# Optimization experiments

Hardware: AMD Instinct MI355X
Metric: run time of the kernel (lower is better)

## Reference

```python
import jax, jax.numpy as jnp
import numpy as np

NUM_HEADS = 16


def spike(x):
    # forward of SpikeFunction: Heaviside step
    return (x > 0).astype(x.dtype)


def setup_inputs() -> dict:
    key = jax.random.key(0)
    ks = jax.random.split(key, 11)
    B, S, D = 2, 2048, 1024
    s = 1.0 / np.sqrt(D)
    return {
        "query": jax.random.normal(ks[0], (B, S, D), jnp.float32),
        "key": jax.random.normal(ks[1], (B, S, D), jnp.float32),
        "value": jax.random.normal(ks[2], (B, S, D), jnp.float32),
        "Wq": jax.random.normal(ks[3], (D, D), jnp.float32) * s,
        "bq": jnp.zeros((D,), jnp.float32),
        "Wk": jax.random.normal(ks[4], (D, D), jnp.float32) * s,
        "bk": jnp.zeros((D,), jnp.float32),
        "Wv": jax.random.normal(ks[5], (D, D), jnp.float32) * s,
        "bv": jnp.zeros((D,), jnp.float32),
        "Wo": jax.random.normal(ks[6], (D, D), jnp.float32) * s,
        "bo": jnp.zeros((D,), jnp.float32),
    }


def reference(query, key, value, Wq, bq, Wk, bk, Wv, bv, Wo, bo):
    B, S, D = query.shape
    H = NUM_HEADS
    hd = D // H
    # torch Linear: x @ W.T + b
    q = (query @ Wq.T + bq).reshape(B, S, H, hd).transpose(0, 2, 1, 3)
    k = (key @ Wk.T + bk).reshape(B, S, H, hd).transpose(0, 2, 1, 3)
    v = (value @ Wv.T + bv).reshape(B, S, H, hd).transpose(0, 2, 1, 3)
    scale = 1.0 / np.sqrt(hd).astype(np.float32)
    scores = jnp.einsum('bhqd,bhkd->bhqk', q, k) * scale  # [B,H,S,S]
    attn = spike(scores)  # elementwise threshold instead of softmax
    ctx = jnp.einsum('bhqk,bhkd->bhqd', attn, v)
    ctx = ctx.transpose(0, 2, 1, 3).reshape(B, S, D)
    out = ctx @ Wo.T + bo
    return out, attn
```

## Files before the change

### kernel.cpp

```cpp
#include <hip/hip_runtime.h>


#define SEQ 2048
#define DIM 1024
#define NH 16
#define HD 64
#define BATCH 2
#define MROWS (BATCH * SEQ)
#define BHT (BATCH * NH)

typedef __attribute__((ext_vector_type(8))) short short8;
typedef __attribute__((ext_vector_type(4))) float f4;
typedef unsigned short ushort;

__device__ __forceinline__ f4 mfma16(short8 a, short8 b, f4 c) {
    return __builtin_amdgcn_mfma_f32_16x16x32_bf16(a, b, c, 0, 0, 0);
}
__device__ __forceinline__ ushort rne16(float x) {
    union { float f; unsigned u; } a; a.f = x;
    return (ushort)((a.u + 0x7fffu + ((a.u >> 16) & 1u)) >> 16);
}
__device__ __forceinline__ void split2(float x, ushort& h, ushort& l) {
    union { float f; unsigned u; } a; a.f = x;
    unsigned hu = a.u & 0xffff0000u;
    h = (ushort)(hu >> 16);
    union { unsigned u; float f; } hb; hb.u = hu;
    l = rne16(x - hb.f);
}
__device__ __forceinline__ short8 ld8(const ushort* p) { return *(const short8*)p; }

__device__ __forceinline__ void gll16(const ushort* g, ushort* l) {
    __builtin_amdgcn_global_load_lds((const __attribute__((address_space(1))) void*)g,
                                     (__attribute__((address_space(3))) void*)l, 16, 0, 0);
}

__global__ __launch_bounds__(256) void wconv(const float* __restrict__ Wq,
                                             const float* __restrict__ Wk,
                                             const float* __restrict__ Wv,
                                             const float* __restrict__ Wo,
                                             ushort* __restrict__ Wqh, ushort* __restrict__ Wql,
                                             ushort* __restrict__ Wkh, ushort* __restrict__ Wkl,
                                             ushort* __restrict__ Wvb, ushort* __restrict__ Wob) {
    int i = (blockIdx.x * 256 + threadIdx.x) * 4;
    int job = blockIdx.y;
    const float* src = job == 0 ? Wq : job == 1 ? Wk : job == 2 ? Wv : Wo;
    float4 w = *(const float4*)&src[i];
    float xs[4] = {w.x, w.y, w.z, w.w};
    if (job < 2) {
        ushort h[4], l[4];
#pragma unroll
        for (int j = 0; j < 4; ++j) split2(xs[j], h[j], l[j]);
        ushort* ph = job ? Wkh : Wqh;
        ushort* pl = job ? Wkl : Wql;
        *(short4*)&ph[i] = make_short4(h[0], h[1], h[2], h[3]);
        *(short4*)&pl[i] = make_short4(l[0], l[1], l[2], l[3]);
    } else {
        ushort* po = job == 2 ? Wvb : Wob;
        *(short4*)&po[i] = make_short4(rne16(xs[0]), rne16(xs[1]), rne16(xs[2]), rne16(xs[3]));
    }
}

template <int B>
__device__ __forceinline__ void ld_qk(const float* __restrict__ X, const ushort* __restrict__ Wh,
                                      const ushort* __restrict__ Wl, int m0, int n0, int la, int qd,
                                      int k0, float4 (&xA)[2][2][2], short8 (&wH)[2][4],
                                      short8 (&wL)[2][4]) {
#pragma unroll
    for (int ms = 0; ms < 2; ++ms) {
        const float* ap = &X[(size_t)(m0 + ms * 16 + la) * DIM + k0 + qd * 8];
        xA[B][ms][0] = *(const float4*)ap;
        xA[B][ms][1] = *(const float4*)(ap + 4);
    }
#pragma unroll
    for (int ns = 0; ns < 4; ++ns) {
        size_t wi = (size_t)(n0 + ns * 16 + la) * DIM + k0 + qd * 8;
        wH[B][ns] = ld8(&Wh[wi]);
        wL[B][ns] = ld8(&Wl[wi]);
    }
}

template <int B>
__device__ __forceinline__ void fma_qk(float4 (&xA)[2][2][2], short8 (&wH)[2][4],
                                       short8 (&wL)[2][4], f4 (&acc)[2][4]) {
    short8 ahi[2], alo[2];
#pragma unroll
    for (int ms = 0; ms < 2; ++ms) {
        float xs[8] = {xA[B][ms][0].x, xA[B][ms][0].y, xA[B][ms][0].z, xA[B][ms][0].w,
                       xA[B][ms][1].x, xA[B][ms][1].y, xA[B][ms][1].z, xA[B][ms][1].w};
#pragma unroll
        for (int j = 0; j < 8; ++j) {
            ushort h, l;
            split2(xs[j], h, l);
            ahi[ms][j] = (short)h;
            alo[ms][j] = (short)l;
        }
    }
#pragma unroll
    for (int ns = 0; ns < 4; ++ns)
#pragma unroll
        for (int ms = 0; ms < 2; ++ms) {
            acc[ms][ns] = mfma16(alo[ms], wH[B][ns], acc[ms][ns]);
            acc[ms][ns] = mfma16(ahi[ms], wL[B][ns], acc[ms][ns]);
            acc[ms][ns] = mfma16(ahi[ms], wH[B][ns], acc[ms][ns]);
        }
}

template <int B>
__device__ __forceinline__ void ld_v(const float* __restrict__ X, const ushort* __restrict__ Wb,
                                     int m0, int n0, int la, int qd, int k0,
                                     float4 (&xA)[2][2][2], short8 (&wH)[2][4]) {
#pragma unroll
    for (int ms = 0; ms < 2; ++ms) {
        const float* ap = &X[(size_t)(m0 + ms * 16 + la) * DIM + k0 + qd * 8];
        xA[B][ms][0] = *(const float4*)ap;
        xA[B][ms][1] = *(const float4*)(ap + 4);
    }
#pragma unroll
    for (int ns = 0; ns < 4; ++ns)
        wH[B][ns] = ld8(&Wb[(size_t)(n0 + ns * 16 + la) * DIM + k0 + qd * 8]);
}

template <int B>
__device__ __forceinline__ void fma_v(float4 (&xA)[2][2][2], short8 (&wH)[2][4], f4 (&acc)[2][4]) {
    short8 a[2];
#pragma unroll
    for (int ms = 0; ms < 2; ++ms) {
        float xs[8] = {xA[B][ms][0].x, xA[B][ms][0].y, xA[B][ms][0].z, xA[B][ms][0].w,
                       xA[B][ms][1].x, xA[B][ms][1].y, xA[B][ms][1].z, xA[B][ms][1].w};
#pragma unroll
        for (int j = 0; j < 8; ++j) a[ms][j] = (short)rne16(xs[j]);
    }
#pragma unroll
    for (int ns = 0; ns < 4; ++ns)
#pragma unroll
        for (int ms = 0; ms < 2; ++ms) acc[ms][ns] = mfma16(a[ms], wH[B][ns], acc[ms][ns]);
}

__global__ __launch_bounds__(256, 2) void proj_qkv(
    const float* __restrict__ query, const float* __restrict__ key, const float* __restrict__ value,
    const ushort* __restrict__ Wqh, const ushort* __restrict__ Wql,
    const ushort* __restrict__ Wkh, const ushort* __restrict__ Wkl,
    const ushort* __restrict__ Wvb,
    const float* __restrict__ bq, const float* __restrict__ bk, const float* __restrict__ bv,
    ushort* __restrict__ Qhi, ushort* __restrict__ Qlo,
    ushort* __restrict__ Khi, ushort* __restrict__ Klo, ushort* __restrict__ Vt) {
    const int z = blockIdx.z;
    const int t = threadIdx.x, wave = t >> 6, lane = t & 63;
    const int la = lane & 15, qd = lane >> 4;
    const int m0 = blockIdx.x * 128 + wave * 32;
    const int n0 = blockIdx.y * 64;

    float4 xA[2][2][2];
    short8 wH[2][4], wL[2][4];
    f4 acc[2][4] = {};

    if (z < 2) {
        const float* X = z ? key : query;
        const ushort* Wh = z ? Wkh : Wqh;
        const ushort* Wl = z ? Wkl : Wql;
        ld_qk<0>(X, Wh, Wl, m0, n0, la, qd, 0, xA, wH, wL);
        for (int k0 = 0; k0 < DIM; k0 += 64) {
            ld_qk<1>(X, Wh, Wl, m0, n0, la, qd, k0 + 32, xA, wH, wL);
            fma_qk<0>(xA, wH, wL, acc);
            ld_qk<0>(X, Wh, Wl, m0, n0, la, qd, (k0 + 64) & (DIM - 1), xA, wH, wL);
            fma_qk<1>(xA, wH, wL, acc);
        }
        const float* bias = z ? bk : bq;
        ushort* Oh = z ? Khi : Qhi;
        ushort* Ol = z ? Klo : Qlo;
#pragma unroll
        for (int ns = 0; ns < 4; ++ns) {
            int n = n0 + ns * 16 + la;
            float bvv = bias[n];
            int h = n >> 6, d = n & 63;
#pragma unroll
            for (int ms = 0; ms < 2; ++ms)
#pragma unroll
                for (int r = 0; r < 4; ++r) {
                    int m = m0 + ms * 16 + qd * 4 + r;
                    int b = m >> 11, s = m & 2047;
                    ushort hh, ll;
                    split2(acc[ms][ns][r] + bvv, hh, ll);
                    size_t o = ((size_t)(b * NH + h) * SEQ + s) * HD + d;
                    __builtin_nontemporal_store(hh, &Oh[o]);
                    __builtin_nontemporal_store(ll, &Ol[o]);
                }
        }
    } else {
        __shared__ ushort Ts[4][64][40];
        ld_v<0>(value, Wvb, m0, n0, la, qd, 0, xA, wH);
        for (int k0 = 0; k0 < DIM; k0 += 64) {
            ld_v<1>(value, Wvb, m0, n0, la, qd, k0 + 32, xA, wH);
            fma_v<0>(xA, wH, acc);
            ld_v<0>(value, Wvb, m0, n0, la, qd, (k0 + 64) & (DIM - 1), xA, wH);
            fma_v<1>(xA, wH, acc);
        }
#pragma unroll
        for (int ns = 0; ns < 4; ++ns) {
            float bvv = bv[n0 + ns * 16 + la];
#pragma unroll
            for (int ms = 0; ms < 2; ++ms)
#pragma unroll
                for (int r = 0; r < 4; ++r)
                    Ts[wave][ns * 16 + la][ms * 16 + qd * 4 + r] = rne16(acc[ms][ns][r] + bvv);
        }
        int b = m0 >> 11, s0 = m0 & 2047, h = n0 >> 6;
        size_t vbase = (size_t)(b * NH + h) * HD * SEQ;
#pragma unroll
        for (int it = 0; it < 4; ++it) {
            int d = it * 16 + (lane >> 2), sc = (lane & 3) * 8;
            short8 v0 = *(const short8*)&Ts[wave][d][sc];
            __builtin_nontemporal_store(v0, (short8*)&Vt[vbase + (size_t)d * SEQ + s0 + sc]);
        }
    }
}

__global__ __launch_bounds__(256, 4) void attn_mfma(
    const ushort* __restrict__ Qhi, const ushort* __restrict__ Qlo,
    const ushort* __restrict__ Khi, const ushort* __restrict__ Klo,
    const ushort* __restrict__ Vt, float* __restrict__ attn, ushort* __restrict__ ctxb) {
    __shared__ ushort kb[2][2][32][64];
    __shared__ ushort Ps[64][40];
    const int t = threadIdx.x, wave = t >> 6, lane = t & 63;
    const int la = lane & 15, qd = lane >> 4;
    const int bh = blockIdx.x;
    const int q0 = blockIdx.y * 64 + wave * 16;

    short8 qhi[2], qlo[2];
#pragma unroll
    for (int ks = 0; ks < 2; ++ks) {
        size_t qi = ((size_t)bh * SEQ + q0 + la) * HD + ks * 32 + qd * 8;
        qhi[ks] = ld8(&Qhi[qi]);
        qlo[ks] = ld8(&Qlo[qi]);
    }

    const int skey = wave * 8 + (lane >> 3);
    const int schunk = (lane & 7) ^ (lane >> 3);
    const size_t sgbase = ((size_t)bh * SEQ + skey) * HD + schunk * 8;

    gll16(&Khi[sgbase], &kb[0][0][wave * 8][0]);
    gll16(&Klo[sgbase], &kb[0][1][wave * 8][0]);
    __syncthreads();

    f4 cacc[4] = {};
    for (int h = 0; h < 64; ++h) {
        const int c0 = h * 32;
        const int cur = h & 1;

        short8 vB[4];
#pragma unroll
        for (int ns = 0; ns < 4; ++ns)
            vB[ns] = ld8(&Vt[((size_t)bh * HD + ns * 16 + la) * SEQ + c0 + qd * 8]);

        if (h + 1 < 64) {
            gll16(&Khi[sgbase + (size_t)(c0 + 32) * HD], &kb[cur ^ 1][0][wave * 8][0]);
            gll16(&Klo[sgbase + (size_t)(c0 + 32) * HD], &kb[cur ^ 1][1][wave * 8][0]);
        }

        short8 kH[2][2], kL[2][2];
#pragma unroll
        for (int n2 = 0; n2 < 2; ++n2)
#pragma unroll
            for (int ks = 0; ks < 2; ++ks) {
                int row = n2 * 16 + la;
                int sw = ((ks * 4 + qd) ^ (la & 7)) * 8;
                kH[n2][ks] = *(const short8*)&kb[cur][0][row][sw];
                kL[n2][ks] = *(const short8*)&kb[cur][1][row][sw];
            }

        f4 s[2] = {};
        __builtin_amdgcn_s_setprio(1);
#pragma unroll
        for (int n2 = 0; n2 < 2; ++n2)
#pragma unroll
            for (int ks = 0; ks < 2; ++ks) {
                s[n2] = mfma16(qlo[ks], kH[n2][ks], s[n2]);
                s[n2] = mfma16(qhi[ks], kL[n2][ks], s[n2]);
                s[n2] = mfma16(qhi[ks], kH[n2][ks], s[n2]);
            }
        __builtin_amdgcn_s_setprio(0);

#pragma unroll
        for (int n2 = 0; n2 < 2; ++n2)
#pragma unroll
            for (int r = 0; r < 4; ++r)
                Ps[wave * 16 + qd * 4 + r][n2 * 16 + la] =
                    s[n2][r] > 0.f ? (ushort)0x3f80 : (ushort)0;

#pragma unroll
        for (int it = 0; it < 2; ++it) {
            int row = it * 8 + (lane >> 3);
            short4 p = *(const short4*)&Ps[wave * 16 + row][(lane & 7) * 4];
            f4 o;
            o.x = __uint_as_float(((unsigned)(ushort)p.x) << 16);
            o.y = __uint_as_float(((unsigned)(ushort)p.y) << 16);
            o.z = __uint_as_float(((unsigned)(ushort)p.z) << 16);
            o.w = __uint_as_float(((unsigned)(ushort)p.w) << 16);
            __builtin_nontemporal_store(
                o, (f4*)&attn[((size_t)bh * SEQ + q0 + row) * SEQ + c0 + (lane & 7) * 4]);
        }

        short8 pa = *(const short8*)&Ps[wave * 16 + la][qd * 8];
        __builtin_amdgcn_s_setprio(1);
#pragma unroll
        for (int ns = 0; ns < 4; ++ns) cacc[ns] = mfma16(pa, vB[ns], cacc[ns]);
        __builtin_amdgcn_s_setprio(0);

        __syncthreads();
    }
#pragma unroll
    for (int ns = 0; ns < 4; ++ns)
#pragma unroll
        for (int r = 0; r < 4; ++r) {
            int qrow = q0 + qd * 4 + r;
            __builtin_nontemporal_store(rne16(cacc[ns][r]),
                                        &ctxb[((size_t)bh * SEQ + qrow) * HD + ns * 16 + la]);
        }
}

template <int B>
__device__ __forceinline__ void ld_o(const ushort* __restrict__ Ctx, const ushort* __restrict__ Wb,
                                     int m0, int n0, int la, int qd, int k0,
                                     short8 (&aO)[2][2], short8 (&wO)[2][4]) {
#pragma unroll
    for (int ms = 0; ms < 2; ++ms) {
        int m = m0 + ms * 16 + la;
        int b = m >> 11, s = m & 2047;
        int k = k0 + qd * 8;
        int h = k >> 6, d = k & 63;
        aO[B][ms] = ld8(&Ctx[((size_t)(b * NH + h) * SEQ + s) * HD + d]);
    }
#pragma unroll
    for (int ns = 0; ns < 4; ++ns)
        wO[B][ns] = ld8(&Wb[(size_t)(n0 + ns * 16 + la) * DIM + k0 + qd * 8]);
}

__global__ __launch_bounds__(256, 2) void proj_out(const ushort* __restrict__ Ctx,
                                                   const ushort* __restrict__ Wb,
                                                   const float* __restrict__ bias,
                                                   float* __restrict__ out) {
    const int t = threadIdx.x, wave = t >> 6, lane = t & 63;
    const int la = lane & 15, qd = lane >> 4;
    const int m0 = blockIdx.x * 128 + wave * 32;
    const int n0 = blockIdx.y * 64;

    short8 aO[2][2], wO[2][4];
    f4 acc[2][4] = {};
    ld_o<0>(Ctx, Wb, m0, n0, la, qd, 0, aO, wO);
    for (int k0 = 0; k0 < DIM; k0 += 64) {
        ld_o<1>(Ctx, Wb, m0, n0, la, qd, k0 + 32, aO, wO);
#pragma unroll
        for (int ns = 0; ns < 4; ++ns)
#pragma unroll
            for (int ms = 0; ms < 2; ++ms) acc[ms][ns] = mfma16(aO[0][ms], wO[0][ns], acc[ms][ns]);
        ld_o<0>(Ctx, Wb, m0, n0, la, qd, (k0 + 64) & (DIM - 1), aO, wO);
#pragma unroll
        for (int ns = 0; ns < 4; ++ns)
#pragma unroll
            for (int ms = 0; ms < 2; ++ms) acc[ms][ns] = mfma16(aO[1][ms], wO[1][ns], acc[ms][ns]);
    }
#pragma unroll
    for (int ns = 0; ns < 4; ++ns) {
        int n = n0 + ns * 16 + la;
        float bvv = bias[n];
#pragma unroll
        for (int ms = 0; ms < 2; ++ms)
#pragma unroll
            for (int r = 0; r < 4; ++r) {
                int m = m0 + ms * 16 + qd * 4 + r;
                __builtin_nontemporal_store(acc[ms][ns][r] + bvv, &out[(size_t)m * DIM + n]);
            }
    }
}

extern "C" void kernel_launch(void* const* d_in, const int* in_sizes, int n_in,
                              void* d_out, int out_size, void* d_ws, size_t ws_size,
                              hipStream_t stream) {
    const float* query = (const float*)d_in[0];
    const float* key   = (const float*)d_in[1];
    const float* value = (const float*)d_in[2];
    const float* Wq = (const float*)d_in[3];
    const float* bq = (const float*)d_in[4];
    const float* Wk = (const float*)d_in[5];
    const float* bk = (const float*)d_in[6];
    const float* Wv = (const float*)d_in[7];
    const float* bv = (const float*)d_in[8];
    const float* Wo = (const float*)d_in[9];
    const float* bo = (const float*)d_in[10];

    float* out  = (float*)d_out;
    float* attn = out + (size_t)MROWS * DIM;

    const size_t NE = (size_t)MROWS * DIM;
    const size_t WE = (size_t)DIM * DIM;
    ushort* Qhi = (ushort*)d_ws;
    ushort* Qlo = Qhi + NE;
    ushort* Khi = Qlo + NE;
    ushort* Klo = Khi + NE;
    ushort* Vt  = Klo + NE;
    ushort* Wqh = Vt + NE;
    ushort* Wql = Wqh + WE;
    ushort* Wkh = Wql + WE;
    ushort* Wkl = Wkh + WE;
    ushort* Wvb = Wkl + WE;
    ushort* Wob = Wvb + WE;
    ushort* Ctx = Wqh;

    dim3 blk(256);
    hipLaunchKernelGGL(wconv, dim3(WE / 1024, 4), blk, 0, stream,
                       Wq, Wk, Wv, Wo, Wqh, Wql, Wkh, Wkl, Wvb, Wob);
    hipLaunchKernelGGL(proj_qkv, dim3(32, 16, 3), blk, 0, stream,
                       query, key, value, Wqh, Wql, Wkh, Wkl, Wvb, bq, bk, bv,
                       Qhi, Qlo, Khi, Klo, Vt);
    hipLaunchKernelGGL(attn_mfma, dim3(32, 32), blk, 0, stream,
                       Qhi, Qlo, Khi, Klo, Vt, attn, Ctx);
    hipLaunchKernelGGL(proj_out, dim3(32, 16), blk, 0, stream, Ctx, Wob, bo, out);
}
```

Before: 1.021 ms.

## Process 64 keys per barrier in attention and shrink output projection tiles

```diff
diff --git a/kernel.cpp b/kernel.cpp
--- a/kernel.cpp
+++ b/kernel.cpp
@@ -219,7 +219,7 @@
     const ushort* __restrict__ Qhi, const ushort* __restrict__ Qlo,
     const ushort* __restrict__ Khi, const ushort* __restrict__ Klo,
     const ushort* __restrict__ Vt, float* __restrict__ attn, ushort* __restrict__ ctxb) {
-    __shared__ ushort kb[2][2][32][64];
+    __shared__ ushort kb[2][2][64][64];
     __shared__ ushort Ps[64][40];
     const int t = threadIdx.x, wave = t >> 6, lane = t & 63;
     const int la = lane & 15, qd = lane >> 4;
@@ -234,77 +234,89 @@
         qlo[ks] = ld8(&Qlo[qi]);
     }
 
-    const int skey = wave * 8 + (lane >> 3);
+    const int skey = wave * 16 + (lane >> 3);
     const int schunk = (lane & 7) ^ (lane >> 3);
-    const size_t sgbase = ((size_t)bh * SEQ + skey) * HD + schunk * 8;
-
-    gll16(&Khi[sgbase], &kb[0][0][wave * 8][0]);
-    gll16(&Klo[sgbase], &kb[0][1][wave * 8][0]);
+    const size_t sg0 = ((size_t)bh * SEQ + skey) * HD + schunk * 8;
+
+    gll16(&Khi[sg0], &kb[0][0][wave * 16][0]);
+    gll16(&Khi[sg0 + 8 * HD], &kb[0][0][wave * 16 + 8][0]);
+    gll16(&Klo[sg0], &kb[0][1][wave * 16][0]);
+    gll16(&Klo[sg0 + 8 * HD], &kb[0][1][wave * 16 + 8][0]);
     __syncthreads();
 
     f4 cacc[4] = {};
-    for (int h = 0; h < 64; ++h) {
-        const int c0 = h * 32;
-        const int cur = h & 1;
-
-        short8 vB[4];
-#pragma unroll
-        for (int ns = 0; ns < 4; ++ns)
-            vB[ns] = ld8(&Vt[((size_t)bh * HD + ns * 16 + la) * SEQ + c0 + qd * 8]);
-
-        if (h + 1 < 64) {
-            gll16(&Khi[sgbase + (size_t)(c0 + 32) * HD], &kb[cur ^ 1][0][wave * 8][0]);
-            gll16(&Klo[sgbase + (size_t)(c0 + 32) * HD], &kb[cur ^ 1][1][wave * 8][0]);
-        }
-
-        short8 kH[2][2], kL[2][2];
-#pragma unroll
-        for (int n2 = 0; n2 < 2; ++n2)
-#pragma unroll
-            for (int ks = 0; ks < 2; ++ks) {
-                int row = n2 * 16 + la;
-                int sw = ((ks * 4 + qd) ^ (la & 7)) * 8;
-                kH[n2][ks] = *(const short8*)&kb[cur][0][row][sw];
-                kL[n2][ks] = *(const short8*)&kb[cur][1][row][sw];
+    for (int h2 = 0; h2 < 32; ++h2) {
+        const int cur = h2 & 1;
+        const int kc = h2 * 64;
+
+        short8 vB[2][4];
+#pragma unroll
+        for (int hf = 0; hf < 2; ++hf)
+#pragma unroll
+            for (int ns = 0; ns < 4; ++ns)
+                vB[hf][ns] =
+                    ld8(&Vt[((size_t)bh * HD + ns * 16 + la) * SEQ + kc + hf * 32 + qd * 8]);
+
+        if (h2 + 1 < 32) {
+            const size_t sn = sg0 + (size_t)(kc + 64) * HD;
+            gll16(&Khi[sn], &kb[cur ^ 1][0][wave * 16][0]);
+            gll16(&Khi[sn + 8 * HD], &kb[cur ^ 1][0][wave * 16 + 8][0]);
+            gll16(&Klo[sn], &kb[cur ^ 1][1][wave * 16][0]);
+            gll16(&Klo[sn + 8 * HD], &kb[cur ^ 1][1][wave * 16 + 8][0]);
+        }
+
+#pragma unroll
+        for (int hf = 0; hf < 2; ++hf) {
+            const int c0 = kc + hf * 32;
+            short8 kH[2][2], kL[2][2];
+#pragma unroll
+            for (int n2 = 0; n2 < 2; ++n2)
+#pragma unroll
+                for (int ks = 0; ks < 2; ++ks) {
+                    int row = (hf * 2 + n2) * 16 + la;
+                    int sw = ((ks * 4 + qd) ^ (la & 7)) * 8;
+                    kH[n2][ks] = *(const short8*)&kb[cur][0][row][sw];
+                    kL[n2][ks] = *(const short8*)&kb[cur][1][row][sw];
+                }
+
+            f4 s[2] = {};
+            __builtin_amdgcn_s_setprio(1);
+#pragma unroll
+            for (int n2 = 0; n2 < 2; ++n2)
+#pragma unroll
+                for (int ks = 0; ks < 2; ++ks) {
+                    s[n2] = mfma16(qlo[ks], kH[n2][ks], s[n2]);
+                    s[n2] = mfma16(qhi[ks], kL[n2][ks], s[n2]);
+                    s[n2] = mfma16(qhi[ks], kH[n2][ks], s[n2]);
+                }
+            __builtin_amdgcn_s_setprio(0);
+
+#pragma unroll
+            for (int n2 = 0; n2 < 2; ++n2)
+#pragma unroll
+                for (int r = 0; r < 4; ++r)
+                    Ps[wave * 16 + qd * 4 + r][n2 * 16 + la] =
+                        s[n2][r] > 0.f ? (ushort)0x3f80 : (ushort)0;
+
+#pragma unroll
+            for (int it = 0; it < 2; ++it) {
+                int row = it * 8 + (lane >> 3);
+                short4 p = *(const short4*)&Ps[wave * 16 + row][(lane & 7) * 4];
+                f4 o;
+                o.x = __uint_as_float(((unsigned)(ushort)p.x) << 16);
+                o.y = __uint_as_float(((unsigned)(ushort)p.y) << 16);
+                o.z = __uint_as_float(((unsigned)(ushort)p.z) << 16);
+                o.w = __uint_as_float(((unsigned)(ushort)p.w) << 16);
+                __builtin_nontemporal_store(
+                    o, (f4*)&attn[((size_t)bh * SEQ + q0 + row) * SEQ + c0 + (lane & 7) * 4]);
             }
 
-        f4 s[2] = {};
-        __builtin_amdgcn_s_setprio(1);
-#pragma unroll
-        for (int n2 = 0; n2 < 2; ++n2)
-#pragma unroll
-            for (int ks = 0; ks < 2; ++ks) {
-                s[n2] = mfma16(qlo[ks], kH[n2][ks], s[n2]);
-                s[n2] = mfma16(qhi[ks], kL[n2][ks], s[n2]);
-                s[n2] = mfma16(qhi[ks], kH[n2][ks], s[n2]);
-            }
-        __builtin_amdgcn_s_setprio(0);
-
-#pragma unroll
-        for (int n2 = 0; n2 < 2; ++n2)
-#pragma unroll
-            for (int r = 0; r < 4; ++r)
-                Ps[wave * 16 + qd * 4 + r][n2 * 16 + la] =
-                    s[n2][r] > 0.f ? (ushort)0x3f80 : (ushort)0;
-
-#pragma unroll
-        for (int it = 0; it < 2; ++it) {
-            int row = it * 8 + (lane >> 3);
-            short4 p = *(const short4*)&Ps[wave * 16 + row][(lane & 7) * 4];
-            f4 o;
-            o.x = __uint_as_float(((unsigned)(ushort)p.x) << 16);
-            o.y = __uint_as_float(((unsigned)(ushort)p.y) << 16);
-            o.z = __uint_as_float(((unsigned)(ushort)p.z) << 16);
-            o.w = __uint_as_float(((unsigned)(ushort)p.w) << 16);
-            __builtin_nontemporal_store(
-                o, (f4*)&attn[((size_t)bh * SEQ + q0 + row) * SEQ + c0 + (lane & 7) * 4]);
-        }
-
-        short8 pa = *(const short8*)&Ps[wave * 16 + la][qd * 8];
-        __builtin_amdgcn_s_setprio(1);
-#pragma unroll
-        for (int ns = 0; ns < 4; ++ns) cacc[ns] = mfma16(pa, vB[ns], cacc[ns]);
-        __builtin_amdgcn_s_setprio(0);
+            short8 pa = *(const short8*)&Ps[wave * 16 + la][qd * 8];
+            __builtin_amdgcn_s_setprio(1);
+#pragma unroll
+            for (int ns = 0; ns < 4; ++ns) cacc[ns] = mfma16(pa, vB[hf][ns], cacc[ns]);
+            __builtin_amdgcn_s_setprio(0);
+        }
 
         __syncthreads();
     }
@@ -321,55 +333,48 @@
 template <int B>
 __device__ __forceinline__ void ld_o(const ushort* __restrict__ Ctx, const ushort* __restrict__ Wb,
                                      int m0, int n0, int la, int qd, int k0,
-                                     short8 (&aO)[2][2], short8 (&wO)[2][4]) {
-#pragma unroll
-    for (int ms = 0; ms < 2; ++ms) {
-        int m = m0 + ms * 16 + la;
+                                     short8 (&aO)[2], short8 (&wO)[2][4]) {
+    {
+        int m = m0 + la;
         int b = m >> 11, s = m & 2047;
         int k = k0 + qd * 8;
         int h = k >> 6, d = k & 63;
-        aO[B][ms] = ld8(&Ctx[((size_t)(b * NH + h) * SEQ + s) * HD + d]);
+        aO[B] = ld8(&Ctx[((size_t)(b * NH + h) * SEQ + s) * HD + d]);
     }
 #pragma unroll
     for (int ns = 0; ns < 4; ++ns)
         wO[B][ns] = ld8(&Wb[(size_t)(n0 + ns * 16 + la) * DIM + k0 + qd * 8]);
 }
 
-__global__ __launch_bounds__(256, 2) void proj_out(const ushort* __restrict__ Ctx,
+__global__ __launch_bounds__(256, 4) void proj_out(const ushort* __restrict__ Ctx,
                                                    const ushort* __restrict__ Wb,
                                                    const float* __restrict__ bias,
                                                    float* __restrict__ out) {
     const int t = threadIdx.x, wave = t >> 6, lane = t & 63;
     const int la = lane & 15, qd = lane >> 4;
-    const int m0 = blockIdx.x * 128 + wave * 32;
+    const int m0 = blockIdx.x * 64 + wave * 16;
     const int n0 = blockIdx.y * 64;
 
-    short8 aO[2][2], wO[2][4];
-    f4 acc[2][4] = {};
+    short8 aO[2], wO[2][4];
+    f4 acc[4] = {};
     ld_o<0>(Ctx, Wb, m0, n0, la, qd, 0, aO, wO);
     for (int k0 = 0; k0 < DIM; k0 += 64) {
         ld_o<1>(Ctx, Wb, m0, n0, la, qd, k0 + 32, aO, wO);
 #pragma unroll
-        for (int ns = 0; ns < 4; ++ns)
-#pragma unroll
-            for (int ms = 0; ms < 2; ++ms) acc[ms][ns] = mfma16(aO[0][ms], wO[0][ns], acc[ms][ns]);
+        for (int ns = 0; ns < 4; ++ns) acc[ns] = mfma16(aO[0], wO[0][ns], acc[ns]);
         ld_o<0>(Ctx, Wb, m0, n0, la, qd, (k0 + 64) & (DIM - 1), aO, wO);
 #pragma unroll
-        for (int ns = 0; ns < 4; ++ns)
-#pragma unroll
-            for (int ms = 0; ms < 2; ++ms) acc[ms][ns] = mfma16(aO[1][ms], wO[1][ns], acc[ms][ns]);
+        for (int ns = 0; ns < 4; ++ns) acc[ns] = mfma16(aO[1], wO[1][ns], acc[ns]);
     }
 #pragma unroll
     for (int ns = 0; ns < 4; ++ns) {
         int n = n0 + ns * 16 + la;
         float bvv = bias[n];
 #pragma unroll
-        for (int ms = 0; ms < 2; ++ms)
-#pragma unroll
-            for (int r = 0; r < 4; ++r) {
-                int m = m0 + ms * 16 + qd * 4 + r;
-                __builtin_nontemporal_store(acc[ms][ns][r] + bvv, &out[(size_t)m * DIM + n]);
-            }
+        for (int r = 0; r < 4; ++r) {
+            int m = m0 + qd * 4 + r;
+            __builtin_nontemporal_store(acc[ns][r] + bvv, &out[(size_t)m * DIM + n]);
+        }
     }
 }
 
@@ -414,5 +419,5 @@
                        Qhi, Qlo, Khi, Klo, Vt);
     hipLaunchKernelGGL(attn_mfma, dim3(32, 32), blk, 0, stream,
                        Qhi, Qlo, Khi, Klo, Vt, attn, Ctx);
-    hipLaunchKernelGGL(proj_out, dim3(32, 16), blk, 0, stream, Ctx, Wob, bo, out);
-}
+    hipLaunchKernelGGL(proj_out, dim3(64, 16), blk, 0, stream, Ctx, Wob, bo, out);
+}
```

Result: slower. 1.052 ms (+3.0%).

## Stage projection weight tiles in shared memory with async double-buffered loads

Applied to the files above, without the earlier changes.

```diff
diff --git a/kernel.cpp b/kernel.cpp
--- a/kernel.cpp
+++ b/kernel.cpp
@@ -60,82 +60,6 @@
     }
 }
 
-template <int B>
-__device__ __forceinline__ void ld_qk(const float* __restrict__ X, const ushort* __restrict__ Wh,
-                                      const ushort* __restrict__ Wl, int m0, int n0, int la, int qd,
-                                      int k0, float4 (&xA)[2][2][2], short8 (&wH)[2][4],
-                                      short8 (&wL)[2][4]) {
-#pragma unroll
-    for (int ms = 0; ms < 2; ++ms) {
-        const float* ap = &X[(size_t)(m0 + ms * 16 + la) * DIM + k0 + qd * 8];
-        xA[B][ms][0] = *(const float4*)ap;
-        xA[B][ms][1] = *(const float4*)(ap + 4);
-    }
-#pragma unroll
-    for (int ns = 0; ns < 4; ++ns) {
-        size_t wi = (size_t)(n0 + ns * 16 + la) * DIM + k0 + qd * 8;
-        wH[B][ns] = ld8(&Wh[wi]);
-        wL[B][ns] = ld8(&Wl[wi]);
-    }
-}
-
-template <int B>
-__device__ __forceinline__ void fma_qk(float4 (&xA)[2][2][2], short8 (&wH)[2][4],
-                                       short8 (&wL)[2][4], f4 (&acc)[2][4]) {
-    short8 ahi[2], alo[2];
-#pragma unroll
-    for (int ms = 0; ms < 2; ++ms) {
-        float xs[8] = {xA[B][ms][0].x, xA[B][ms][0].y, xA[B][ms][0].z, xA[B][ms][0].w,
-                       xA[B][ms][1].x, xA[B][ms][1].y, xA[B][ms][1].z, xA[B][ms][1].w};
-#pragma unroll
-        for (int j = 0; j < 8; ++j) {
-            ushort h, l;
-            split2(xs[j], h, l);
-            ahi[ms][j] = (short)h;
-            alo[ms][j] = (short)l;
-        }
-    }
-#pragma unroll
-    for (int ns = 0; ns < 4; ++ns)
-#pragma unroll
-        for (int ms = 0; ms < 2; ++ms) {
-            acc[ms][ns] = mfma16(alo[ms], wH[B][ns], acc[ms][ns]);
-            acc[ms][ns] = mfma16(ahi[ms], wL[B][ns], acc[ms][ns]);
-            acc[ms][ns] = mfma16(ahi[ms], wH[B][ns], acc[ms][ns]);
-        }
-}
-
-template <int B>
-__device__ __forceinline__ void ld_v(const float* __restrict__ X, const ushort* __restrict__ Wb,
-                                     int m0, int n0, int la, int qd, int k0,
-                                     float4 (&xA)[2][2][2], short8 (&wH)[2][4]) {
-#pragma unroll
-    for (int ms = 0; ms < 2; ++ms) {
-        const float* ap = &X[(size_t)(m0 + ms * 16 + la) * DIM + k0 + qd * 8];
-        xA[B][ms][0] = *(const float4*)ap;
-        xA[B][ms][1] = *(const float4*)(ap + 4);
-    }
-#pragma unroll
-    for (int ns = 0; ns < 4; ++ns)
-        wH[B][ns] = ld8(&Wb[(size_t)(n0 + ns * 16 + la) * DIM + k0 + qd * 8]);
-}
-
-template <int B>
-__device__ __forceinline__ void fma_v(float4 (&xA)[2][2][2], short8 (&wH)[2][4], f4 (&acc)[2][4]) {
-    short8 a[2];
-#pragma unroll
-    for (int ms = 0; ms < 2; ++ms) {
-        float xs[8] = {xA[B][ms][0].x, xA[B][ms][0].y, xA[B][ms][0].z, xA[B][ms][0].w,
-                       xA[B][ms][1].x, xA[B][ms][1].y, xA[B][ms][1].z, xA[B][ms][1].w};
-#pragma unroll
-        for (int j = 0; j < 8; ++j) a[ms][j] = (short)rne16(xs[j]);
-    }
-#pragma unroll
-    for (int ns = 0; ns < 4; ++ns)
-#pragma unroll
-        for (int ms = 0; ms < 2; ++ms) acc[ms][ns] = mfma16(a[ms], wH[B][ns], acc[ms][ns]);
-}
-
 __global__ __launch_bounds__(256, 2) void proj_qkv(
     const float* __restrict__ query, const float* __restrict__ key, const float* __restrict__ value,
     const ushort* __restrict__ Wqh, const ushort* __restrict__ Wql,
@@ -144,26 +68,78 @@
     const float* __restrict__ bq, const float* __restrict__ bk, const float* __restrict__ bv,
     ushort* __restrict__ Qhi, ushort* __restrict__ Qlo,
     ushort* __restrict__ Khi, ushort* __restrict__ Klo, ushort* __restrict__ Vt) {
+    __shared__ ushort wst[2][2][64][64];
+    __shared__ ushort Ts[4][64][40];
     const int z = blockIdx.z;
     const int t = threadIdx.x, wave = t >> 6, lane = t & 63;
     const int la = lane & 15, qd = lane >> 4;
     const int m0 = blockIdx.x * 128 + wave * 32;
     const int n0 = blockIdx.y * 64;
 
-    float4 xA[2][2][2];
-    short8 wH[2][4], wL[2][4];
-    f4 acc[2][4] = {};
+    const int srow = wave * 16 + (lane >> 3);
+    const int schunk = (lane & 7) ^ (lane >> 3);
+    const size_t wg0 = (size_t)(n0 + srow) * DIM + schunk * 8;
 
     if (z < 2) {
         const float* X = z ? key : query;
         const ushort* Wh = z ? Wkh : Wqh;
         const ushort* Wl = z ? Wkl : Wql;
-        ld_qk<0>(X, Wh, Wl, m0, n0, la, qd, 0, xA, wH, wL);
+
+        gll16(&Wh[wg0], &wst[0][0][wave * 16][0]);
+        gll16(&Wh[wg0 + 8 * DIM], &wst[0][0][wave * 16 + 8][0]);
+        gll16(&Wl[wg0], &wst[0][1][wave * 16][0]);
+        gll16(&Wl[wg0 + 8 * DIM], &wst[0][1][wave * 16 + 8][0]);
+        __syncthreads();
+
+        f4 acc[2][4] = {};
         for (int k0 = 0; k0 < DIM; k0 += 64) {
-            ld_qk<1>(X, Wh, Wl, m0, n0, la, qd, k0 + 32, xA, wH, wL);
-            fma_qk<0>(xA, wH, wL, acc);
-            ld_qk<0>(X, Wh, Wl, m0, n0, la, qd, (k0 + 64) & (DIM - 1), xA, wH, wL);
-            fma_qk<1>(xA, wH, wL, acc);
+            const int cur = (k0 >> 6) & 1;
+            float4 xA[2][2][2];
+#pragma unroll
+            for (int hf = 0; hf < 2; ++hf)
+#pragma unroll
+                for (int ms = 0; ms < 2; ++ms) {
+                    const float* ap = &X[(size_t)(m0 + ms * 16 + la) * DIM + k0 + hf * 32 + qd * 8];
+                    xA[hf][ms][0] = *(const float4*)ap;
+                    xA[hf][ms][1] = *(const float4*)(ap + 4);
+                }
+            if (k0 + 64 < DIM) {
+                gll16(&Wh[wg0 + k0 + 64], &wst[cur ^ 1][0][wave * 16][0]);
+                gll16(&Wh[wg0 + k0 + 64 + 8 * DIM], &wst[cur ^ 1][0][wave * 16 + 8][0]);
+                gll16(&Wl[wg0 + k0 + 64], &wst[cur ^ 1][1][wave * 16][0]);
+                gll16(&Wl[wg0 + k0 + 64 + 8 * DIM], &wst[cur ^ 1][1][wave * 16 + 8][0]);
+            }
+#pragma unroll
+            for (int hf = 0; hf < 2; ++hf) {
+                short8 ahi[2], alo[2];
+#pragma unroll
+                for (int ms = 0; ms < 2; ++ms) {
+                    float xs[8] = {xA[hf][ms][0].x, xA[hf][ms][0].y, xA[hf][ms][0].z,
+                                   xA[hf][ms][0].w, xA[hf][ms][1].x, xA[hf][ms][1].y,
+                                   xA[hf][ms][1].z, xA[hf][ms][1].w};
+#pragma unroll
+                    for (int j = 0; j < 8; ++j) {
+                        ushort h, l;
+                        split2(xs[j], h, l);
+                        ahi[ms][j] = (short)h;
+                        alo[ms][j] = (short)l;
+                    }
+                }
+#pragma unroll
+                for (int ns = 0; ns < 4; ++ns) {
+                    int row = ns * 16 + la;
+                    int sw = ((hf * 4 + qd) ^ (la & 7)) * 8;
+                    short8 wHf = *(const short8*)&wst[cur][0][row][sw];
+                    short8 wLf = *(const short8*)&wst[cur][1][row][sw];
+#pragma unroll
+                    for (int ms = 0; ms < 2; ++ms) {
+                        acc[ms][ns] = mfma16(alo[ms], wHf, acc[ms][ns]);
+                        acc[ms][ns] = mfma16(ahi[ms], wLf, acc[ms][ns]);
+                        acc[ms][ns] = mfma16(ahi[ms], wHf, acc[ms][ns]);
+                    }
+                }
+            }
+            __syncthreads();
         }
         const float* bias = z ? bk : bq;
         ushort* Oh = z ? Khi : Qhi;
@@ -187,13 +163,48 @@
                 }
         }
     } else {
-        __shared__ ushort Ts[4][64][40];
-        ld_v<0>(value, Wvb, m0, n0, la, qd, 0, xA, wH);
+        gll16(&Wvb[wg0], &wst[0][0][wave * 16][0]);
+        gll16(&Wvb[wg0 + 8 * DIM], &wst[0][0][wave * 16 + 8][0]);
+        __syncthreads();
+
+        f4 acc[2][4] = {};
         for (int k0 = 0; k0 < DIM; k0 += 64) {
-            ld_v<1>(value, Wvb, m0, n0, la, qd, k0 + 32, xA, wH);
-            fma_v<0>(xA, wH, acc);
-            ld_v<0>(value, Wvb, m0, n0, la, qd, (k0 + 64) & (DIM - 1), xA, wH);
-            fma_v<1>(xA, wH, acc);
+            const int cur = (k0 >> 6) & 1;
+            float4 xA[2][2][2];
+#pragma unroll
+            for (int hf = 0; hf < 2; ++hf)
+#pragma unroll
+                for (int ms = 0; ms < 2; ++ms) {
+                    const float* ap =
+                        &value[(size_t)(m0 + ms * 16 + la) * DIM + k0 + hf * 32 + qd * 8];
+                    xA[hf][ms][0] = *(const float4*)ap;
+                    xA[hf][ms][1] = *(const float4*)(ap + 4);
+                }
+            if (k0 + 64 < DIM) {
+                gll16(&Wvb[wg0 + k0 + 64], &wst[cur ^ 1][0][wave * 16][0]);
+                gll16(&Wvb[wg0 + k0 + 64 + 8 * DIM], &wst[cur ^ 1][0][wave * 16 + 8][0]);
+            }
+#pragma unroll
+            for (int hf = 0; hf < 2; ++hf) {
+                short8 a[2];
+#pragma unroll
+                for (int ms = 0; ms < 2; ++ms) {
+                    float xs[8] = {xA[hf][ms][0].x, xA[hf][ms][0].y, xA[hf][ms][0].z,
+                                   xA[hf][ms][0].w, xA[hf][ms][1].x, xA[hf][ms][1].y,
+                                   xA[hf][ms][1].z, xA[hf][ms][1].w};
+#pragma unroll
+                    for (int j = 0; j < 8; ++j) a[ms][j] = (short)rne16(xs[j]);
+                }
+#pragma unroll
+                for (int ns = 0; ns < 4; ++ns) {
+                    int row = ns * 16 + la;
+                    int sw = ((hf * 4 + qd) ^ (la & 7)) * 8;
+                    short8 wv = *(const short8*)&wst[cur][0][row][sw];
+#pragma unroll
+                    for (int ms = 0; ms < 2; ++ms) acc[ms][ns] = mfma16(a[ms], wv, acc[ms][ns]);
+                }
+            }
+            __syncthreads();
         }
 #pragma unroll
         for (int ns = 0; ns < 4; ++ns) {
```

Measured after the change: 903.2 us. -11.6%, faster.
